# Kernel optimization log

Hardware: AMD Instinct MI355X
Metric: run time of the kernel (lower is better)

## Reference

```python
import jax, jax.numpy as jnp
import numpy as np

TOKENS = 8192
D_IN = 4096
D_OUT = 4096


def setup_inputs() -> dict:
    key = jax.random.key(0)
    k1, k2, k3 = jax.random.split(key, 3)
    input = jax.random.normal(k1, (TOKENS, D_IN), dtype=jnp.float32)
    # int8 quantized weight, stored here as int32 (stand-in for torch.int8 buffer)
    weight = jax.random.randint(k2, (D_OUT, D_IN), -127, 127, dtype=jnp.int32)
    # per-output-channel dequant scales
    scales = jax.random.uniform(k3, (D_OUT,), dtype=jnp.float32) * 0.02
    return {"input": input, "weight": weight, "scales": scales}


def reference(input, weight, scales):
    # F.linear(input, weight.to(input.dtype), bias=False) * scales
    w = weight.astype(input.dtype)            # dequantize to input dtype
    out = jnp.einsum('ti,oi->to', input, w)   # [tokens, out_features]
    return out * scales.astype(input.dtype)   # per-channel scale
```

## Files before the change

kernel.cpp:

```cpp
#include <hip/hip_runtime.h>
#include <hip/hip_bf16.h>

typedef __bf16 bf16;
typedef __bf16 bf16x4 __attribute__((ext_vector_type(4)));
typedef __bf16 bf16x8 __attribute__((ext_vector_type(8)));
typedef float  f32x4  __attribute__((ext_vector_type(4)));

#define M_DIM 8192
#define N_DIM 4096
#define K_DIM 4096

#define GLOBAL_AS __attribute__((address_space(1)))
#define LDS_AS    __attribute__((address_space(3)))


__global__ __launch_bounds__(256) void cvt_input_bf16(const float4* __restrict__ in,
                                                      bf16x8* __restrict__ out) {
    int idx = blockIdx.x * 256 + threadIdx.x;
    float4 v0 = in[2 * idx];
    float4 v1 = in[2 * idx + 1];
    bf16x8 o;
    o[0] = (bf16)v0.x; o[1] = (bf16)v0.y; o[2] = (bf16)v0.z; o[3] = (bf16)v0.w;
    o[4] = (bf16)v1.x; o[5] = (bf16)v1.y; o[6] = (bf16)v1.z; o[7] = (bf16)v1.w;
    out[idx] = o;
}

__global__ __launch_bounds__(256) void cvt_weight_bf16(const int4* __restrict__ in,
                                                       bf16x8* __restrict__ out) {
    int idx = blockIdx.x * 256 + threadIdx.x;
    int4 v0 = in[2 * idx];
    int4 v1 = in[2 * idx + 1];
    bf16x8 o;
    o[0] = (bf16)(float)v0.x; o[1] = (bf16)(float)v0.y;
    o[2] = (bf16)(float)v0.z; o[3] = (bf16)(float)v0.w;
    o[4] = (bf16)(float)v1.x; o[5] = (bf16)(float)v1.y;
    o[6] = (bf16)(float)v1.z; o[7] = (bf16)(float)v1.w;
    out[idx] = o;
}


__global__ __launch_bounds__(256, 2) void gemm_bt_bf16(const bf16* __restrict__ A,
                                                       const bf16* __restrict__ B,
                                                       const float* __restrict__ scales,
                                                       float* __restrict__ C) {
    __shared__ bf16 lds_a[128 * 32];
    __shared__ bf16 lds_b[128 * 32];

    const int tid  = threadIdx.x;
    const int wave = tid >> 6;
    const int lane = tid & 63;
    const int m0 = blockIdx.y * 128;
    const int n0 = blockIdx.x * 128;
    const int wm = (wave >> 1) * 64;
    const int wn = (wave & 1) * 64;

    const int srow0 = tid >> 2;
    const int scol  = (((tid & 3) ^ ((tid >> 3) & 3))) * 8;

    const int la = lane & 15;
    const int lk = (((lane >> 4) ^ ((la >> 1) & 3))) * 8;

    f32x4 acc[4][4] = {};

    for (int k0 = 0; k0 < K_DIM; k0 += 32) {
        __syncthreads();
#pragma unroll
        for (int i = 0; i < 2; ++i) {
            const int row = srow0 + i * 64;
            const bf16* gp = A + (size_t)(m0 + row) * K_DIM + k0 + scol;
            __builtin_amdgcn_global_load_lds((GLOBAL_AS const void*)gp,
                                             (LDS_AS void*)(lds_a + row * 32 + (tid & 3) * 8),
                                             16, 0, 0);
        }
#pragma unroll
        for (int i = 0; i < 2; ++i) {
            const int row = srow0 + i * 64;
            const bf16* gp = B + (size_t)(n0 + row) * K_DIM + k0 + scol;
            __builtin_amdgcn_global_load_lds((GLOBAL_AS const void*)gp,
                                             (LDS_AS void*)(lds_b + row * 32 + (tid & 3) * 8),
                                             16, 0, 0);
        }
        __syncthreads();

        bf16x8 af[4], bfg[4];
#pragma unroll
        for (int i = 0; i < 4; ++i)
            af[i] = *(const bf16x8*)(lds_a + (wm + i * 16 + la) * 32 + lk);
#pragma unroll
        for (int j = 0; j < 4; ++j)
            bfg[j] = *(const bf16x8*)(lds_b + (wn + j * 16 + la) * 32 + lk);
#pragma unroll
        for (int i = 0; i < 4; ++i)
#pragma unroll
            for (int j = 0; j < 4; ++j)
                acc[i][j] = __builtin_amdgcn_mfma_f32_16x16x32_bf16(af[i], bfg[j], acc[i][j], 0, 0, 0);
    }

    const int crow = (lane >> 4) * 4;
#pragma unroll
    for (int j = 0; j < 4; ++j) {
        const int col = n0 + wn + j * 16 + la;
        const float s = scales[col];
#pragma unroll
        for (int i = 0; i < 4; ++i) {
            const int rowb = m0 + wm + i * 16 + crow;
#pragma unroll
            for (int r = 0; r < 4; ++r)
                C[(size_t)(rowb + r) * N_DIM + col] = acc[i][j][r] * s;
        }
    }
}


__global__ __launch_bounds__(256, 2) void gemm_fused(const float* __restrict__ A,
                                                     const int* __restrict__ B,
                                                     const float* __restrict__ scales,
                                                     float* __restrict__ C) {
    __shared__ bf16 lds_a[128 * 32];
    __shared__ bf16 lds_b[128 * 32];

    const int tid  = threadIdx.x;
    const int wave = tid >> 6;
    const int lane = tid & 63;
    const int m0 = blockIdx.y * 128;
    const int n0 = blockIdx.x * 128;
    const int wm = (wave >> 1) * 64;
    const int wn = (wave & 1) * 64;

    const int sr = tid >> 1;
    const int sc = (tid & 1) * 16;

    const int la = lane & 15;
    const int lk = (lane >> 4) * 8;

    f32x4 acc[4][4] = {};

    for (int k0 = 0; k0 < K_DIM; k0 += 32) {
        __syncthreads();
        {
            const float* ga = A + (size_t)(m0 + sr) * K_DIM + k0 + sc;
            float4 v0 = *(const float4*)(ga + 0);
            float4 v1 = *(const float4*)(ga + 4);
            float4 v2 = *(const float4*)(ga + 8);
            float4 v3 = *(const float4*)(ga + 12);
            bf16x8 p0, p1;
            p0[0]=(bf16)v0.x; p0[1]=(bf16)v0.y; p0[2]=(bf16)v0.z; p0[3]=(bf16)v0.w;
            p0[4]=(bf16)v1.x; p0[5]=(bf16)v1.y; p0[6]=(bf16)v1.z; p0[7]=(bf16)v1.w;
            p1[0]=(bf16)v2.x; p1[1]=(bf16)v2.y; p1[2]=(bf16)v2.z; p1[3]=(bf16)v2.w;
            p1[4]=(bf16)v3.x; p1[5]=(bf16)v3.y; p1[6]=(bf16)v3.z; p1[7]=(bf16)v3.w;
            *(bf16x8*)(lds_a + sr * 32 + sc)     = p0;
            *(bf16x8*)(lds_a + sr * 32 + sc + 8) = p1;
        }
        {
            const int* gb = B + (size_t)(n0 + sr) * K_DIM + k0 + sc;
            int4 v0 = *(const int4*)(gb + 0);
            int4 v1 = *(const int4*)(gb + 4);
            int4 v2 = *(const int4*)(gb + 8);
            int4 v3 = *(const int4*)(gb + 12);
            bf16x8 p0, p1;
            p0[0]=(bf16)(float)v0.x; p0[1]=(bf16)(float)v0.y; p0[2]=(bf16)(float)v0.z; p0[3]=(bf16)(float)v0.w;
            p0[4]=(bf16)(float)v1.x; p0[5]=(bf16)(float)v1.y; p0[6]=(bf16)(float)v1.z; p0[7]=(bf16)(float)v1.w;
            p1[0]=(bf16)(float)v2.x; p1[1]=(bf16)(float)v2.y; p1[2]=(bf16)(float)v2.z; p1[3]=(bf16)(float)v2.w;
            p1[4]=(bf16)(float)v3.x; p1[5]=(bf16)(float)v3.y; p1[6]=(bf16)(float)v3.z; p1[7]=(bf16)(float)v3.w;
            *(bf16x8*)(lds_b + sr * 32 + sc)     = p0;
            *(bf16x8*)(lds_b + sr * 32 + sc + 8) = p1;
        }
        __syncthreads();

        bf16x8 af[4], bfg[4];
#pragma unroll
        for (int i = 0; i < 4; ++i)
            af[i] = *(const bf16x8*)(lds_a + (wm + i * 16 + la) * 32 + lk);
#pragma unroll
        for (int j = 0; j < 4; ++j)
            bfg[j] = *(const bf16x8*)(lds_b + (wn + j * 16 + la) * 32 + lk);
#pragma unroll
        for (int i = 0; i < 4; ++i)
#pragma unroll
            for (int j = 0; j < 4; ++j)
                acc[i][j] = __builtin_amdgcn_mfma_f32_16x16x32_bf16(af[i], bfg[j], acc[i][j], 0, 0, 0);
    }

    const int crow = (lane >> 4) * 4;
#pragma unroll
    for (int j = 0; j < 4; ++j) {
        const int col = n0 + wn + j * 16 + la;
        const float s = scales[col];
#pragma unroll
        for (int i = 0; i < 4; ++i) {
            const int rowb = m0 + wm + i * 16 + crow;
#pragma unroll
            for (int r = 0; r < 4; ++r)
                C[(size_t)(rowb + r) * N_DIM + col] = acc[i][j][r] * s;
        }
    }
}


extern "C" void kernel_launch(void* const* d_in, const int* in_sizes, int n_in,
                              void* d_out, int out_size, void* d_ws, size_t ws_size,
                              hipStream_t stream) {
    const float* input  = (const float*)d_in[0];
    const int*   weight = (const int*)d_in[1];
    const float* scales = (const float*)d_in[2];
    float* out = (float*)d_out;

    const size_t needA = (size_t)M_DIM * K_DIM * sizeof(bf16);
    const size_t needB = (size_t)N_DIM * K_DIM * sizeof(bf16);

    dim3 grid(N_DIM / 128, M_DIM / 128);

    if (ws_size >= needA + needB) {
        bf16* Abf = (bf16*)d_ws;
        bf16* Bbf = (bf16*)((char*)d_ws + needA);
        cvt_input_bf16<<<(M_DIM * (size_t)K_DIM / 8) / 256, 256, 0, stream>>>(
            (const float4*)input, (bf16x8*)Abf);
        cvt_weight_bf16<<<(N_DIM * (size_t)K_DIM / 8) / 256, 256, 0, stream>>>(
            (const int4*)weight, (bf16x8*)Bbf);
        gemm_bt_bf16<<<grid, 256, 0, stream>>>(Abf, Bbf, scales, out);
    } else {
        gemm_fused<<<grid, 256, 0, stream>>>(input, weight, scales, out);
    }
}
```

Measured before the change: 568.9 us.

## Replace bf16 GEMM with 256x256 tile, 8-wave, double-buffered pipelined kernel

Replaces the 128x128, 4-wave, single-buffered bf16 GEMM with a 256x256 tile kernel using 512 threads, BK=64 and double-buffered LDS. Global-to-LDS loads for upcoming k-steps are interleaved with MFMA blocks under explicit barriers, waitcnts and setprio. The grid index is swizzled so neighbouring blocks share data in L2. The goal is to raise arithmetic intensity and hide load latency, at the cost of 128KB LDS per block, which limits occupancy, plus fragile hand scheduling.

```diff
diff --git a/kernel.cpp b/kernel.cpp
--- a/kernel.cpp
+++ b/kernel.cpp
@@ -2,13 +2,13 @@
 #include <hip/hip_bf16.h>
 
 typedef __bf16 bf16;
-typedef __bf16 bf16x4 __attribute__((ext_vector_type(4)));
 typedef __bf16 bf16x8 __attribute__((ext_vector_type(8)));
 typedef float  f32x4  __attribute__((ext_vector_type(4)));
 
 #define M_DIM 8192
 #define N_DIM 4096
 #define K_DIM 4096
+#define NT    (K_DIM / 64)
 
 #define GLOBAL_AS __attribute__((address_space(1)))
 #define LDS_AS    __attribute__((address_space(3)))
@@ -39,76 +39,160 @@
 }
 
 
-__global__ __launch_bounds__(256, 2) void gemm_bt_bf16(const bf16* __restrict__ A,
-                                                       const bf16* __restrict__ B,
-                                                       const float* __restrict__ scales,
-                                                       float* __restrict__ C) {
-    __shared__ bf16 lds_a[128 * 32];
-    __shared__ bf16 lds_b[128 * 32];
+__global__ __launch_bounds__(512, 2) void gemm_bt_256(const bf16* __restrict__ A,
+                                                      const bf16* __restrict__ B,
+                                                      const float* __restrict__ scales,
+                                                      float* __restrict__ C) {
+    __shared__ bf16 ldsA[2 * 16384];
+    __shared__ bf16 ldsB[2 * 16384];
 
     const int tid  = threadIdx.x;
     const int wave = tid >> 6;
     const int lane = tid & 63;
-    const int m0 = blockIdx.y * 128;
-    const int n0 = blockIdx.x * 128;
-    const int wm = (wave >> 1) * 64;
-    const int wn = (wave & 1) * 64;
-
-    const int srow0 = tid >> 2;
-    const int scol  = (((tid & 3) ^ ((tid >> 3) & 3))) * 8;
-
-    const int la = lane & 15;
-    const int lk = (((lane >> 4) ^ ((la >> 1) & 3))) * 8;
-
-    f32x4 acc[4][4] = {};
-
-    for (int k0 = 0; k0 < K_DIM; k0 += 32) {
-        __syncthreads();
-#pragma unroll
-        for (int i = 0; i < 2; ++i) {
-            const int row = srow0 + i * 64;
-            const bf16* gp = A + (size_t)(m0 + row) * K_DIM + k0 + scol;
-            __builtin_amdgcn_global_load_lds((GLOBAL_AS const void*)gp,
-                                             (LDS_AS void*)(lds_a + row * 32 + (tid & 3) * 8),
-                                             16, 0, 0);
-        }
-#pragma unroll
-        for (int i = 0; i < 2; ++i) {
-            const int row = srow0 + i * 64;
-            const bf16* gp = B + (size_t)(n0 + row) * K_DIM + k0 + scol;
-            __builtin_amdgcn_global_load_lds((GLOBAL_AS const void*)gp,
-                                             (LDS_AS void*)(lds_b + row * 32 + (tid & 3) * 8),
-                                             16, 0, 0);
-        }
-        __syncthreads();
-
-        bf16x8 af[4], bfg[4];
-#pragma unroll
-        for (int i = 0; i < 4; ++i)
-            af[i] = *(const bf16x8*)(lds_a + (wm + i * 16 + la) * 32 + lk);
-#pragma unroll
-        for (int j = 0; j < 4; ++j)
-            bfg[j] = *(const bf16x8*)(lds_b + (wn + j * 16 + la) * 32 + lk);
-#pragma unroll
-        for (int i = 0; i < 4; ++i)
-#pragma unroll
-            for (int j = 0; j < 4; ++j)
-                acc[i][j] = __builtin_amdgcn_mfma_f32_16x16x32_bf16(af[i], bfg[j], acc[i][j], 0, 0, 0);
-    }
-
-    const int crow = (lane >> 4) * 4;
+    const int wm   = wave >> 2;
+    const int wn   = wave & 3;
+
+    const int wg  = blockIdx.x;
+    const int swz = (wg & 7) * (512 >> 3) + (wg >> 3);
+    const int n0  = (swz & 15) * 256;
+    const int m0  = (swz >> 4) * 256;
+
+    const int sr = tid >> 3;
+    const int sc = ((tid & 7) ^ (sr & 7)) * 8;
+    const int so = tid * 8;
+
+    const int la15 = lane & 15;
+    const int lhi  = lane >> 4;
+    const int rlow = la15 & 7;
+    const int ck0  = ((lhi) ^ rlow) * 8;
+    const int ck1  = ((4 + lhi) ^ rlow) * 8;
+    const int wrA  = wm * 128;
+    const int wrB  = wn * 64;
+
+    f32x4  acc[8][4] = {};
+    bf16x8 af[2][4], b0[2][2], b1[2][2];
+
+#define STAGE_A(KT, H) do {                                                              \
+    const int _kk = (KT) & (NT - 1);                                                     \
+    const int _bb = ((KT) & 1) * 16384;                                                  \
+    const bf16* _g0 = A + (size_t)(m0 + (H) * 128 + sr) * K_DIM + _kk * 64 + sc;         \
+    __builtin_amdgcn_global_load_lds((GLOBAL_AS const void*)_g0,                         \
+        (LDS_AS void*)(ldsA + _bb + (H) * 8192 + so), 16, 0, 0);                         \
+    const bf16* _g1 = A + (size_t)(m0 + (H) * 128 + 64 + sr) * K_DIM + _kk * 64 + sc;    \
+    __builtin_amdgcn_global_load_lds((GLOBAL_AS const void*)_g1,                         \
+        (LDS_AS void*)(ldsA + _bb + (H) * 8192 + 4096 + so), 16, 0, 0);                  \
+} while (0)
+
+#define STAGE_B(KT, H) do {                                                              \
+    const int _kk = (KT) & (NT - 1);                                                     \
+    const int _bb = ((KT) & 1) * 16384;                                                  \
+    const bf16* _g0 = B + (size_t)(n0 + (H) * 128 + sr) * K_DIM + _kk * 64 + sc;         \
+    __builtin_amdgcn_global_load_lds((GLOBAL_AS const void*)_g0,                         \
+        (LDS_AS void*)(ldsB + _bb + (H) * 8192 + so), 16, 0, 0);                         \
+    const bf16* _g1 = B + (size_t)(n0 + (H) * 128 + 64 + sr) * K_DIM + _kk * 64 + sc;    \
+    __builtin_amdgcn_global_load_lds((GLOBAL_AS const void*)_g1,                         \
+        (LDS_AS void*)(ldsB + _bb + (H) * 8192 + 4096 + so), 16, 0, 0);                  \
+} while (0)
+
+#define LDA(MH, BO) do {                                                                 \
+    _Pragma("unroll")                                                                    \
+    for (int _i = 0; _i < 4; ++_i) {                                                     \
+        const int _r = (BO) + (wrA + (MH) * 64 + _i * 16 + la15) * 64;                   \
+        af[0][_i] = *(const bf16x8*)(ldsA + _r + ck0);                                   \
+        af[1][_i] = *(const bf16x8*)(ldsA + _r + ck1);                                   \
+    }                                                                                    \
+} while (0)
+
+#define LDB(NH, DST, BO) do {                                                            \
+    _Pragma("unroll")                                                                    \
+    for (int _j = 0; _j < 2; ++_j) {                                                     \
+        const int _r = (BO) + (wrB + (NH) * 32 + _j * 16 + la15) * 64;                   \
+        DST[0][_j] = *(const bf16x8*)(ldsB + _r + ck0);                                  \
+        DST[1][_j] = *(const bf16x8*)(ldsB + _r + ck1);                                  \
+    }                                                                                    \
+} while (0)
+
+#define MMA_BLK(I0, J0, BB) do {                                                         \
+    __builtin_amdgcn_s_setprio(1);                                                       \
+    _Pragma("unroll")                                                                    \
+    for (int _i = 0; _i < 4; ++_i) {                                                     \
+        _Pragma("unroll")                                                                \
+        for (int _j = 0; _j < 2; ++_j) {                                                 \
+            acc[(I0) + _i][(J0) + _j] = __builtin_amdgcn_mfma_f32_16x16x32_bf16(         \
+                af[0][_i], BB[0][_j], acc[(I0) + _i][(J0) + _j], 0, 0, 0);               \
+            acc[(I0) + _i][(J0) + _j] = __builtin_amdgcn_mfma_f32_16x16x32_bf16(         \
+                af[1][_i], BB[1][_j], acc[(I0) + _i][(J0) + _j], 0, 0, 0);               \
+        }                                                                                \
+    }                                                                                    \
+    __builtin_amdgcn_s_setprio(0);                                                       \
+} while (0)
+
+#define BAR()    __builtin_amdgcn_s_barrier()
+#define LGKM0()  do { asm volatile("s_waitcnt lgkmcnt(0)" ::: "memory");                 \
+                      __builtin_amdgcn_sched_barrier(0); } while (0)
+#define SCHED0() __builtin_amdgcn_sched_barrier(0)
+
+    STAGE_A(0, 0); STAGE_B(0, 0); STAGE_A(0, 1); STAGE_B(0, 1);
+    STAGE_B(1, 0); STAGE_A(1, 0);
+    asm volatile("s_waitcnt vmcnt(4)" ::: "memory");
+    BAR(); SCHED0();
+
+    for (int t = 0; t < NT; ++t) {
+        const int bo = (t & 1) * 16384;
+
+        LDA(0, bo);
+        LDB(0, b0, bo);
+        STAGE_A(t + 1, 1);
+        BAR();
+        LGKM0();
+        MMA_BLK(0, 0, b0);
+        BAR(); SCHED0();
+
+        LDB(1, b1, bo);
+        STAGE_B(t + 1, 1);
+        BAR();
+        LGKM0();
+        MMA_BLK(0, 2, b1);
+        BAR(); SCHED0();
+
+        LDA(1, bo);
+        STAGE_B(t + 2, 0);
+        BAR();
+        LGKM0();
+        MMA_BLK(4, 2, b1);
+        BAR(); SCHED0();
+
+        STAGE_A(t + 2, 0);
+        BAR();
+        MMA_BLK(4, 0, b0);
+        asm volatile("s_waitcnt vmcnt(4)" ::: "memory");
+        BAR(); SCHED0();
+    }
+
+    asm volatile("s_waitcnt vmcnt(0)" ::: "memory");
+
+    const int crow = lhi * 4;
 #pragma unroll
     for (int j = 0; j < 4; ++j) {
-        const int col = n0 + wn + j * 16 + la;
+        const int col = n0 + wrB + j * 16 + la15;
         const float s = scales[col];
 #pragma unroll
-        for (int i = 0; i < 4; ++i) {
-            const int rowb = m0 + wm + i * 16 + crow;
+        for (int i = 0; i < 8; ++i) {
+            const int rowb = m0 + wrA + i * 16 + crow;
 #pragma unroll
             for (int r = 0; r < 4; ++r)
                 C[(size_t)(rowb + r) * N_DIM + col] = acc[i][j][r] * s;
         }
     }
+
+#undef STAGE_A
+#undef STAGE_B
+#undef LDA
+#undef LDB
+#undef MMA_BLK
+#undef BAR
+#undef LGKM0
+#undef SCHED0
 }
 
 
@@ -208,8 +292,6 @@
     const size_t needA = (size_t)M_DIM * K_DIM * sizeof(bf16);
     const size_t needB = (size_t)N_DIM * K_DIM * sizeof(bf16);
 
-    dim3 grid(N_DIM / 128, M_DIM / 128);
-
     if (ws_size >= needA + needB) {
         bf16* Abf = (bf16*)d_ws;
         bf16* Bbf = (bf16*)((char*)d_ws + needA);
@@ -217,8 +299,9 @@
             (const float4*)input, (bf16x8*)Abf);
         cvt_weight_bf16<<<(N_DIM * (size_t)K_DIM / 8) / 256, 256, 0, stream>>>(
             (const int4*)weight, (bf16x8*)Bbf);
-        gemm_bt_bf16<<<grid, 256, 0, stream>>>(Abf, Bbf, scales, out);
+        gemm_bt_256<<<(M_DIM / 256) * (N_DIM / 256), 512, 0, stream>>>(Abf, Bbf, scales, out);
     } else {
+        dim3 grid(N_DIM / 128, M_DIM / 128);
         gemm_fused<<<grid, 256, 0, stream>>>(input, weight, scales, out);
     }
 }
```

Result: no change. 565.4 us (-0.6%).
